# Kernel tuning notes

Measured on AMD Instinct MI355X. Metric: run time of the kernel, lower is better.

Reference implementation:

```python
import jax, jax.numpy as jnp
import numpy as np

D_MODEL = 1024
EXPAND = 2
D_INNER = D_MODEL * EXPAND  # 2048
D_STATE = 16
D_CONV = 4
B, T = 4, 2048


def setup_inputs() -> dict:
    key = jax.random.key(0)
    ks = jax.random.split(key, 8)
    s = 0.02  # small init std for numeric stability
    return {
        "x": jax.random.normal(ks[0], (B, T, D_MODEL), jnp.float32),
        "in_proj_w": jax.random.normal(ks[1], (2 * D_INNER, D_MODEL), jnp.float32) * s,
        "conv_w": jax.random.normal(ks[2], (D_INNER, 1, D_CONV), jnp.float32) * s,
        "conv_b": jnp.zeros((D_INNER,), jnp.float32),
        "x_proj_w": jax.random.normal(ks[3], (2 * D_STATE, D_INNER), jnp.float32) * s,
        "dt_proj_w": jax.random.normal(ks[4], (D_INNER, D_STATE), jnp.float32) * s,
        "dt_proj_b": jnp.zeros((D_INNER,), jnp.float32),
        "D_param": jnp.ones((D_INNER,), jnp.float32),
        "out_proj_w": jax.random.normal(ks[5], (D_MODEL, D_INNER), jnp.float32) * s,
    }


def reference(x, in_proj_w, conv_w, conv_b, x_proj_w, dt_proj_w, dt_proj_b, D_param, out_proj_w):
    Bsz, Tlen, _ = x.shape
    # in_proj (no bias), torch Linear: x @ W.T
    xz = jnp.einsum('btd,ed->bte', x, in_proj_w)            # [B,T,2*D_INNER]
    x_inner, z = jnp.split(xz, 2, axis=-1)                   # each [B,T,D_INNER]
    # depthwise causal conv1d: left-pad d_conv-1, take first T outputs
    xc = jnp.transpose(x_inner, (0, 2, 1))                   # [B,D_INNER,T]
    xc = jax.lax.conv_general_dilated(
        xc, conv_w, window_strides=(1,), padding=[(D_CONV - 1, 0)],
        feature_group_count=D_INNER)
    xc = xc + conv_b[None, :, None]
    x_conv = jax.nn.silu(jnp.transpose(xc, (0, 2, 1)))       # [B,T,D_INNER]
    # x_proj -> (B_ssm, C_ssm); C_ssm is unused by the simplified scan (faithful)
    x_ssm = jnp.einsum('btd,ed->bte', x_conv, x_proj_w)      # [B,T,2*D_STATE]
    B_ssm, C_ssm = jnp.split(x_ssm, 2, axis=-1)
    dt = jax.nn.softplus(jnp.einsum('btn,dn->btd', B_ssm, dt_proj_w) + dt_proj_b)  # [B,T,D_INNER]
    # simplified selective scan: EMA with scalar-per-timestep gate
    alpha = jax.nn.sigmoid(jnp.mean(dt, axis=-1, keepdims=True))  # [B,T,1]

    def step(h, inp):
        a, xt = inp
        h = a * h + (1.0 - a) * xt
        return h, h

    aT = jnp.transpose(alpha, (1, 0, 2))   # [T,B,1]
    xT = jnp.transpose(x_conv, (1, 0, 2))  # [T,B,D_INNER]
    h0 = jnp.zeros((Bsz, D_INNER), x.dtype)
    _, ys = jax.lax.scan(step, h0, (aT, xT))
    y = jnp.transpose(ys, (1, 0, 2))        # [B,T,D_INNER]
    y = y * D_param + x_conv                # skip with learned D
    y = y * jax.nn.silu(z)                  # gate
    out = jnp.einsum('btd,ed->bte', y, out_proj_w)  # [B,T,D_MODEL]
    return out
```

## Files before the change

### kernel.cpp

```cpp
#include <hip/hip_runtime.h>
#include <stdint.h>

#define TLEN   2048
#define DMODEL 1024
#define DINNER 2048
#define MROWS  8192
#define NCH    16
#define CHUNK  128

typedef unsigned short u16;
typedef __bf16 bf16x8 __attribute__((ext_vector_type(8)));
typedef float  f32x4  __attribute__((ext_vector_type(4)));

__device__ __forceinline__ float bf2f(u16 u) {
  union { unsigned int i; float f; } v; v.i = ((unsigned int)u) << 16; return v.f;
}
__device__ __forceinline__ u16 f2bf(float f) {
  union { float f; unsigned int u; } v; v.f = f;
  unsigned int u = v.u;
  return (u16)((u + 0x7fffu + ((u >> 16) & 1u)) >> 16);
}
__device__ __forceinline__ float silu_f(float x) { return x / (1.f + __expf(-x)); }

__device__ __forceinline__ void async16(const u16* g, u16* l) {
  __builtin_amdgcn_global_load_lds(
      (const __attribute__((address_space(1))) void*)(g),
      (__attribute__((address_space(3))) void*)(l),
      16, 0, 0);
}

#define BAR      asm volatile("s_barrier" ::: "memory")
#define WAITV(n) asm volatile("s_waitcnt vmcnt(" #n ")" ::: "memory")
#define PRIO1    __builtin_amdgcn_s_setprio(1)
#define PRIO0    __builtin_amdgcn_s_setprio(0)

__global__ __launch_bounds__(256) void k_convert(const float* __restrict__ x,
    const float* __restrict__ w1, const float* __restrict__ w3,
    const float* __restrict__ xpw,
    u16* __restrict__ xb, u16* __restrict__ w1b, u16* __restrict__ w3b,
    u16* __restrict__ xpwb) {
  int i = blockIdx.x * 256 + threadIdx.x;
  const int nx  = MROWS * DMODEL / 4;
  const int nw1 = 2 * DINNER * DMODEL / 4;
  const int nw3 = DMODEL * DINNER / 4;
  const float* src; u16* dst; int j;
  if (i < nx)                  { src = x;   dst = xb;   j = i; }
  else if (i < nx + nw1)       { src = w1;  dst = w1b;  j = i - nx; }
  else if (i < nx + nw1 + nw3) { src = w3;  dst = w3b;  j = i - nx - nw1; }
  else                         { src = xpw; dst = xpwb; j = i - nx - nw1 - nw3; }
  float4 v = ((const float4*)src)[j];
  ushort4 o;
  o.x = f2bf(v.x); o.y = f2bf(v.y); o.z = f2bf(v.z); o.w = f2bf(v.w);
  ((ushort4*)dst)[j] = o;
}

__device__ __forceinline__ u16* regp(u16* lds, int s, int mat, int h) {
  return lds + (((s * 2 + mat) * 2 + h) * 8192);
}

__device__ __forceinline__ void read_a(bf16x8 (&dst)[4][2], const u16* reg,
                                       int qa, int fr, int c0, int c1) {
  #pragma unroll
  for (int m = 0; m < 4; m++) {
    const u16* p = reg + (qa * 64 + m * 16 + fr) * 64;
    dst[m][0] = *(const bf16x8*)(p + c0);
    dst[m][1] = *(const bf16x8*)(p + c1);
  }
}
__device__ __forceinline__ void read_b(bf16x8 (&dst)[2][2], const u16* reg,
                                       int rb, int c0, int c1) {
  #pragma unroll
  for (int n = 0; n < 2; n++) {
    const u16* p = reg + (rb + n * 16) * 64;
    dst[n][0] = *(const bf16x8*)(p + c0);
    dst[n][1] = *(const bf16x8*)(p + c1);
  }
}
__device__ __forceinline__ void mfma_quad(f32x4 (&acc)[8][4],
    const bf16x8 (&af)[4][2], const bf16x8 (&bf)[2][2], int qa, int qb) {
  #pragma unroll
  for (int m = 0; m < 4; m++)
    #pragma unroll
    for (int n = 0; n < 2; n++)
      #pragma unroll
      for (int ks = 0; ks < 2; ks++)
        acc[qa * 4 + m][qb * 2 + n] = __builtin_amdgcn_mfma_f32_16x16x32_bf16(
            af[m][ks], bf[n][ks], acc[qa * 4 + m][qb * 2 + n], 0, 0, 0);
}

template<int N, int K, bool OUT_BF16>
__global__ __launch_bounds__(512) void k_gemm8p(const u16* __restrict__ A,
    const u16* __restrict__ Bm, void* __restrict__ C) {
  static_assert(K % 128 == 0, "K must be multiple of 128");
  extern __shared__ u16 lds[];
  const int tid  = threadIdx.x;
  const int lane = tid & 63;
  const int wave = tid >> 6;
  const int wm   = wave >> 2;
  const int wn   = wave & 3;
  const int fr   = lane & 15;
  const int q    = lane >> 4;

  int wg = blockIdx.x, nwg = gridDim.x, swz = wg;
  if ((nwg & 7) == 0) swz = (wg & 7) * (nwg >> 3) + (wg >> 3);
  const int NT_N = N / 256;
  const size_t blockM = (size_t)(swz / NT_N) * 256;
  const size_t blockN = (size_t)(swz % NT_N) * 256;

  const int rsub   = tid >> 3;
  const int srcCol = 8 * ((tid & 7) ^ (rsub & 7));
  const u16* gA = A  + (blockM + rsub) * (size_t)K + srcCol;
  const u16* gB = Bm + (blockN + rsub) * (size_t)K + srcCol;

#define STAGE(sl, mat, h, kt) do {                                           \
    const u16* _g = ((mat) ? gB : gA) + (size_t)(h) * (128 * (size_t)K)      \
                    + (size_t)(kt) * 64;                                     \
    u16* _l = regp(lds, (sl), (mat), (h)) + tid * 8;                         \
    async16(_g, _l);                                                         \
    async16(_g + (size_t)64 * K, _l + 4096);                                 \
  } while (0)

  const int c0 = (((q * 16)      ^ ((fr & 7) << 4)) >> 1);
  const int c1 = (((64 + q * 16) ^ ((fr & 7) << 4)) >> 1);
  const int rb = (wn & 1) * 64 + fr;

  f32x4 acc[8][4] = {};
  bf16x8 a0[4][2], a1[4][2], bl[2][2], bh[2][2];

  const int NT = K / 64;
  const int NITER = K / 128;

  STAGE(0, 0, 0, 0); STAGE(0, 0, 1, 0); STAGE(0, 1, 0, 0); STAGE(0, 1, 1, 0);
  STAGE(1, 1, 0, 1); STAGE(1, 1, 1, 1); STAGE(1, 0, 0, 1);
  WAITV(6);
  BAR;

  for (int it = 0; it < NITER; ++it) {
    const int t2 = 2 * it + 2, t3 = 2 * it + 3;
    const bool pf = (t2 < NT);
    read_a(a0, regp(lds, 0, 0, wm), 0, fr, c0, c1);
    read_b(bl, regp(lds, 0, 1, wn >> 1), rb, c0, c1);
    STAGE(1, 0, 1, 2 * it + 1);
    BAR;
    PRIO1; mfma_quad(acc, a0, bl, 0, 0); PRIO0;
    BAR;
    read_b(bh, regp(lds, 0, 1, wn >> 1), rb + 32, c0, c1);
    if (pf) STAGE(0, 1, 0, t2);
    BAR;
    PRIO1; mfma_quad(acc, a0, bh, 0, 1); PRIO0;
    BAR;
    read_a(a1, regp(lds, 0, 0, wm), 1, fr, c0, c1);
    if (pf) STAGE(0, 1, 1, t2);
    BAR;
    PRIO1; mfma_quad(acc, a1, bl, 1, 0); PRIO0;
    BAR;
    if (pf) STAGE(0, 0, 0, t2);
    BAR;
    PRIO1; mfma_quad(acc, a1, bh, 1, 1); PRIO0;
    if (pf) { WAITV(6); } else { WAITV(0); }
    BAR;
    read_a(a0, regp(lds, 1, 0, wm), 0, fr, c0, c1);
    read_b(bl, regp(lds, 1, 1, wn >> 1), rb, c0, c1);
    if (pf) STAGE(0, 0, 1, t2);
    BAR;
    PRIO1; mfma_quad(acc, a0, bl, 0, 0); PRIO0;
    BAR;
    read_b(bh, regp(lds, 1, 1, wn >> 1), rb + 32, c0, c1);
    if (pf) STAGE(1, 1, 0, t3);
    BAR;
    PRIO1; mfma_quad(acc, a0, bh, 0, 1); PRIO0;
    BAR;
    read_a(a1, regp(lds, 1, 0, wm), 1, fr, c0, c1);
    if (pf) STAGE(1, 1, 1, t3);
    BAR;
    PRIO1; mfma_quad(acc, a1, bl, 1, 0); PRIO0;
    BAR;
    if (pf) STAGE(1, 0, 0, t3);
    BAR;
    PRIO1; mfma_quad(acc, a1, bh, 1, 1); PRIO0;
    if (pf) { WAITV(6); BAR; } else { BAR; }
  }
#undef STAGE

  {
    const size_t r0  = blockM + (size_t)wm * 128;
    const size_t cc0 = blockN + (size_t)wn * 64;
    #pragma unroll
    for (int m = 0; m < 8; m++)
      #pragma unroll
      for (int n = 0; n < 4; n++)
        #pragma unroll
        for (int r = 0; r < 4; r++) {
          size_t row = r0 + m * 16 + q * 4 + r;
          size_t col = cc0 + n * 16 + fr;
          float v = acc[m][n][r];
          if (OUT_BF16) ((u16*)C)[row * N + col] = f2bf(v);
          else          ((float*)C)[row * N + col] = v;
        }
  }
}

template<int N, int K, bool OUT_BF16>
__global__ __launch_bounds__(256) void k_gemm_bt(const u16* __restrict__ A,
    const u16* __restrict__ B, void* __restrict__ C) {
  __shared__ u16 sA[2][128 * 32];
  __shared__ u16 sB[2][128 * 32];
  const int tid  = threadIdx.x;
  const int lane = tid & 63;
  const int wave = tid >> 6;
  const int wm   = (wave >> 1) * 64;
  const int wn   = (wave & 1) * 64;
  const int fr   = lane & 15;
  const int q    = lane >> 4;
  const size_t blockM = (size_t)blockIdx.y * 128;
  const size_t blockN = (size_t)blockIdx.x * 128;

  const int srow = lane >> 2;
  const int scol = (lane & 3) * 8;
  const u16* gA = A + (blockM + (size_t)wave * 32 + srow) * (size_t)K + scol;
  const u16* gB = B + (blockN + (size_t)wave * 32 + srow) * (size_t)K + scol;
  u16* lA0 = sA[0] + wave * 1024;
  u16* lA1 = sA[1] + wave * 1024;
  u16* lB0 = sB[0] + wave * 1024;
  u16* lB1 = sB[1] + wave * 1024;

  f32x4 acc[4][4] = {};

  for (int kt = 0; kt < K; kt += 64) {
    async16(gA + kt,                        lA0);
    async16(gA + 16 * (size_t)K + kt,       lA0 + 512);
    async16(gA + kt + 32,                   lA1);
    async16(gA + 16 * (size_t)K + kt + 32,  lA1 + 512);
    async16(gB + kt,                        lB0);
    async16(gB + 16 * (size_t)K + kt,       lB0 + 512);
    async16(gB + kt + 32,                   lB1);
    async16(gB + 16 * (size_t)K + kt + 32,  lB1 + 512);
    __syncthreads();

    #pragma unroll
    for (int h = 0; h < 2; h++) {
      bf16x8 af[4], bfr[4];
      #pragma unroll
      for (int tm = 0; tm < 4; tm++)
        af[tm] = *(const bf16x8*)(sA[h] + (wm + tm * 16 + fr) * 32 + q * 8);
      #pragma unroll
      for (int tn = 0; tn < 4; tn++)
        bfr[tn] = *(const bf16x8*)(sB[h] + (wn + tn * 16 + fr) * 32 + q * 8);
      #pragma unroll
      for (int tm = 0; tm < 4; tm++)
        #pragma unroll
        for (int tn = 0; tn < 4; tn++)
          acc[tm][tn] = __builtin_amdgcn_mfma_f32_16x16x32_bf16(
              af[tm], bfr[tn], acc[tm][tn], 0, 0, 0);
    }
    __syncthreads();
  }

  #pragma unroll
  for (int tm = 0; tm < 4; tm++)
    #pragma unroll
    for (int tn = 0; tn < 4; tn++)
      #pragma unroll
      for (int r = 0; r < 4; r++) {
        size_t row = blockM + wm + tm * 16 + q * 4 + r;
        size_t col = blockN + wn + tn * 16 + fr;
        float v = acc[tm][tn][r];
        if (OUT_BF16) ((u16*)C)[row * N + col] = f2bf(v);
        else          ((float*)C)[row * N + col] = v;
      }
}

__global__ __launch_bounds__(256) void k_conv(const u16* __restrict__ xz,
    const float* __restrict__ cw, const float* __restrict__ cb,
    u16* __restrict__ xc) {
  int idx = blockIdx.x * 256 + threadIdx.x;
  int d  = idx & (DINNER - 1);
  int tb = (idx >> 11) & 255;
  int b  = idx >> 19;
  float4 w = ((const float4*)cw)[d];
  float bias = cb[d];
  const u16* inp = xz + ((size_t)(b * TLEN + tb * 8)) * 4096 + d;
  float v[11];
  #pragma unroll
  for (int j = 0; j < 11; j++) {
    int t = tb * 8 - 3 + j;
    v[j] = (t >= 0) ? bf2f(inp[(ptrdiff_t)(j - 3) * 4096]) : 0.f;
  }
  u16* outp = xc + ((size_t)(b * TLEN + tb * 8)) * DINNER + d;
  #pragma unroll
  for (int i = 0; i < 8; i++) {
    float acc = bias + w.x * v[i] + w.y * v[i + 1] + w.z * v[i + 2] + w.w * v[i + 3];
    outp[(size_t)i * DINNER] = f2bf(silu_f(acc));
  }
}

__global__ __launch_bounds__(256) void k_bssm(const u16* __restrict__ xc,
    const u16* __restrict__ xpwb, float* __restrict__ bssm) {
  const int tid  = threadIdx.x;
  const int lane = tid & 63;
  const int wave = tid >> 6;
  const int fr   = lane & 15;
  const int q    = lane >> 4;
  const size_t row0 = (size_t)blockIdx.x * 32;
  const int k0 = wave * 512;

  f32x4 acc[2] = {};
  #pragma unroll
  for (int kk = 0; kk < 512; kk += 32) {
    const int kb = k0 + kk + q * 8;
    bf16x8 bfrag = *(const bf16x8*)(xpwb + (size_t)fr * DINNER + kb);
    #pragma unroll
    for (int tm = 0; tm < 2; tm++) {
      bf16x8 afrag = *(const bf16x8*)(xc + (row0 + tm * 16 + fr) * (size_t)DINNER + kb);
      acc[tm] = __builtin_amdgcn_mfma_f32_16x16x32_bf16(afrag, bfrag, acc[tm], 0, 0, 0);
    }
  }

  __shared__ float red[4][32][16];
  #pragma unroll
  for (int tm = 0; tm < 2; tm++)
    #pragma unroll
    for (int r = 0; r < 4; r++)
      red[wave][tm * 16 + q * 4 + r][fr] = acc[tm][r];
  __syncthreads();
  #pragma unroll
  for (int i = tid; i < 512; i += 256) {
    int r = i >> 4, n = i & 15;
    bssm[(row0 + r) * 16 + n] =
        red[0][r][n] + red[1][r][n] + red[2][r][n] + red[3][r][n];
  }
}

__global__ __launch_bounds__(256) void k_alpha(const float* __restrict__ bssm,
    const float* __restrict__ dtw, const float* __restrict__ dtb,
    float* __restrict__ alpha) {
  const int tid = threadIdx.x;
  const size_t row0 = (size_t)blockIdx.x * 16;
  __shared__ float4 sB[16][4];
  { int r = tid >> 4, n = tid & 15;
    ((float*)&sB[r][0])[n] = bssm[(row0 + r) * 16 + n]; }
  __syncthreads();

  float rowsum[16];
  #pragma unroll
  for (int r = 0; r < 16; r++) rowsum[r] = 0.f;

  #pragma unroll 1
  for (int m = 0; m < 4; m++) {
    const int d0 = m * 512 + tid * 2;
    float4 w[2][4]; float bias[2];
    #pragma unroll
    for (int j = 0; j < 2; j++) {
      const float4* wp = (const float4*)(dtw + (size_t)(d0 + j) * 16);
      w[j][0] = wp[0]; w[j][1] = wp[1]; w[j][2] = wp[2]; w[j][3] = wp[3];
      bias[j] = dtb[d0 + j];
    }
    #pragma unroll
    for (int r = 0; r < 16; r++) {
      float4 b0 = sB[r][0], b1 = sB[r][1], b2 = sB[r][2], b3 = sB[r][3];
      float s = 0.f;
      #pragma unroll
      for (int j = 0; j < 2; j++) {
        float dot = bias[j]
          + b0.x * w[j][0].x + b0.y * w[j][0].y + b0.z * w[j][0].z + b0.w * w[j][0].w
          + b1.x * w[j][1].x + b1.y * w[j][1].y + b1.z * w[j][1].z + b1.w * w[j][1].w
          + b2.x * w[j][2].x + b2.y * w[j][2].y + b2.z * w[j][2].z + b2.w * w[j][2].w
          + b3.x * w[j][3].x + b3.y * w[j][3].y + b3.z * w[j][3].z + b3.w * w[j][3].w;
        s += (dot > 15.f) ? dot : __logf(1.f + __expf(dot));
      }
      rowsum[r] += s;
    }
  }
  #pragma unroll
  for (int r = 0; r < 16; r++)
    #pragma unroll
    for (int off = 32; off > 0; off >>= 1) rowsum[r] += __shfl_xor(rowsum[r], off);
  __shared__ float red[4][16];
  if ((tid & 63) == 0) {
    #pragma unroll
    for (int r = 0; r < 16; r++) red[tid >> 6][r] = rowsum[r];
  }
  __syncthreads();
  if (tid < 16) {
    float mean = (red[0][tid] + red[1][tid] + red[2][tid] + red[3][tid]) * (1.f / DINNER);
    alpha[row0 + tid] = 1.f / (1.f + __expf(-mean));
  }
}

__global__ __launch_bounds__(256) void k_scan1(const u16* __restrict__ xc,
    const float* __restrict__ alpha, float* __restrict__ carry) {
  const int blk = blockIdx.x;
  const int g = blk & 7;
  const int c = (blk >> 3) & 15;
  const int b = blk >> 7;
  const int d = g * 256 + threadIdx.x;
  __shared__ float sa[CHUNK];
  if (threadIdx.x < CHUNK) sa[threadIdx.x] = alpha[b * TLEN + c * CHUNK + threadIdx.x];
  __syncthreads();
  const u16* xp = xc + ((size_t)(b * TLEN + c * CHUNK)) * DINNER + d;
  float h = 0.f;
  #pragma unroll 8
  for (int i = 0; i < CHUNK; i++) {
    float a = sa[i];
    float xv = bf2f(xp[(size_t)i * DINNER]);
    h = a * h + (1.f - a) * xv;
  }
  carry[((size_t)(b * NCH + c)) * DINNER + d] = h;
}

__global__ __launch_bounds__(256) void k_scan2(float* __restrict__ carry,
    const float* __restrict__ alpha) {
  int i = blockIdx.x * 256 + threadIdx.x;
  int b = i >> 11;
  int d = i & (DINNER - 1);
  __shared__ float sP[NCH];
  if (threadIdx.x < NCH) {
    const float* ap = alpha + b * TLEN + threadIdx.x * CHUNK;
    float p = 1.f;
    for (int j = 0; j < CHUNK; j++) p *= ap[j];
    sP[threadIdx.x] = p;
  }
  __syncthreads();
  float h = 0.f;
  #pragma unroll
  for (int c = 0; c < NCH; c++) {
    size_t idx = ((size_t)(b * NCH + c)) * DINNER + d;
    float cv = carry[idx];
    carry[idx] = h;
    h = sP[c] * h + cv;
  }
}

__global__ __launch_bounds__(256) void k_scan3(const u16* __restrict__ xc,
    const u16* __restrict__ xz, const float* __restrict__ alpha,
    const float* __restrict__ Hs, const float* __restrict__ Dp,
    u16* __restrict__ yg) {
  const int blk = blockIdx.x;
  const int g = blk & 7;
  const int c = (blk >> 3) & 15;
  const int b = blk >> 7;
  const int d = g * 256 + threadIdx.x;
  __shared__ float sa[CHUNK];
  if (threadIdx.x < CHUNK) sa[threadIdx.x] = alpha[b * TLEN + c * CHUNK + threadIdx.x];
  __syncthreads();
  float h = Hs[((size_t)(b * NCH + c)) * DINNER + d];
  const float Dv = Dp[d];
  const size_t row0 = (size_t)(b * TLEN + c * CHUNK);
  #pragma unroll 4
  for (int i = 0; i < CHUNK; i++) {
    size_t row = row0 + i;
    float a = sa[i];
    float xv = bf2f(xc[row * DINNER + d]);
    h = a * h + (1.f - a) * xv;
    float zv = bf2f(xz[row * 4096 + DINNER + d]);
    float y = h * Dv + xv;
    yg[row * DINNER + d] = f2bf(y * silu_f(zv));
  }
}

extern "C" void kernel_launch(void* const* d_in, const int* in_sizes, int n_in,
                              void* d_out, int out_size, void* d_ws, size_t ws_size,
                              hipStream_t stream) {
  const float* x   = (const float*)d_in[0];
  const float* w1  = (const float*)d_in[1];
  const float* cw  = (const float*)d_in[2];
  const float* cb  = (const float*)d_in[3];
  const float* xpw = (const float*)d_in[4];
  const float* dtw = (const float*)d_in[5];
  const float* dtb = (const float*)d_in[6];
  const float* Dp  = (const float*)d_in[7];
  const float* w3  = (const float*)d_in[8];
  float* out = (float*)d_out;
  char* ws = (char*)d_ws;

  u16*   xb    = (u16*)(ws + 0);
  u16*   w1b   = (u16*)(ws + 16777216);
  u16*   w3b   = (u16*)(ws + 25165824);
  u16*   xz    = (u16*)(ws + 29360128);
  u16*   xc    = (u16*)(ws + 96468992);
  u16*   yg    = (u16*)(ws + 130023424);
  float* bssm  = (float*)(ws + 163577856);
  float* alpha = (float*)(ws + 164102144);
  float* carry = (float*)(ws + 164135168);
  u16*   xpwb  = (u16*)(ws + 164659456);

  k_convert<<<14368, 256, 0, stream>>>(x, w1, w3, xpw, xb, w1b, w3b, xpwb);
  k_gemm8p<4096, 1024, true><<<512, 512, 131072, stream>>>(xb, w1b, xz);
  k_conv   <<<8192, 256, 0, stream>>>(xz, cw, cb, xc);
  k_bssm   <<<256, 256, 0, stream>>>(xc, xpwb, bssm);
  k_alpha  <<<512, 256, 0, stream>>>(bssm, dtw, dtb, alpha);
  k_scan1  <<<512, 256, 0, stream>>>(xc, alpha, carry);
  k_scan2  <<<32, 256, 0, stream>>>(carry, alpha);
  k_scan3  <<<512, 256, 0, stream>>>(xc, xz, alpha, carry, Dp, yg);
  k_gemm_bt<1024, 2048, false><<<dim3(8, 64), 256, 0, stream>>>(yg, w3b, out);
}
```

Before: 329.8 us.

## Vectorize conv and scan kernels, shorten scan chunks, split-K output GEMM

Conv, scan1 and scan3 now process 8 consecutive channels per thread with 16-byte bf16 loads and stores instead of scalar 2-byte accesses. Scan chunk length shrinks from 128 to 32, giving more chunks and shorter serial chains. The output projection GEMM uses 512 threads with two K halves reduced through shared memory to raise occupancy and latency hiding. The carry buffer is moved to reuse the dead input-conversion region; fewer threads in scans may reduce parallelism.

```diff
diff --git a/kernel.cpp b/kernel.cpp
--- a/kernel.cpp
+++ b/kernel.cpp
@@ -5,8 +5,8 @@
 #define DMODEL 1024
 #define DINNER 2048
 #define MROWS  8192
-#define NCH    16
-#define CHUNK  128
+#define NCH    64
+#define CHUNK  32
 
 typedef unsigned short u16;
 typedef __bf16 bf16x8 __attribute__((ext_vector_type(8)));
@@ -201,32 +201,34 @@
 }
 
 template<int N, int K, bool OUT_BF16>
-__global__ __launch_bounds__(256) void k_gemm_bt(const u16* __restrict__ A,
+__global__ __launch_bounds__(512) void k_gemm_sk(const u16* __restrict__ A,
     const u16* __restrict__ B, void* __restrict__ C) {
-  __shared__ u16 sA[2][128 * 32];
-  __shared__ u16 sB[2][128 * 32];
-  const int tid  = threadIdx.x;
-  const int lane = tid & 63;
-  const int wave = tid >> 6;
-  const int wm   = (wave >> 1) * 64;
-  const int wn   = (wave & 1) * 64;
-  const int fr   = lane & 15;
-  const int q    = lane >> 4;
+  __shared__ u16 smem[2][2][2][4096];
+  const int tid   = threadIdx.x;
+  const int lane  = tid & 63;
+  const int wave8 = tid >> 6;
+  const int kw    = wave8 >> 2;
+  const int wave  = wave8 & 3;
+  const int wm    = (wave >> 1) * 64;
+  const int wn    = (wave & 1) * 64;
+  const int fr    = lane & 15;
+  const int q     = lane >> 4;
   const size_t blockM = (size_t)blockIdx.y * 128;
   const size_t blockN = (size_t)blockIdx.x * 128;
 
   const int srow = lane >> 2;
   const int scol = (lane & 3) * 8;
-  const u16* gA = A + (blockM + (size_t)wave * 32 + srow) * (size_t)K + scol;
-  const u16* gB = B + (blockN + (size_t)wave * 32 + srow) * (size_t)K + scol;
-  u16* lA0 = sA[0] + wave * 1024;
-  u16* lA1 = sA[1] + wave * 1024;
-  u16* lB0 = sB[0] + wave * 1024;
-  u16* lB1 = sB[1] + wave * 1024;
+  const size_t kbase = (size_t)kw * (K / 2);
+  const u16* gA = A + (blockM + (size_t)wave * 32 + srow) * (size_t)K + kbase + scol;
+  const u16* gB = B + (blockN + (size_t)wave * 32 + srow) * (size_t)K + kbase + scol;
+  u16* lA0 = smem[kw][0][0] + wave * 1024;
+  u16* lA1 = smem[kw][0][1] + wave * 1024;
+  u16* lB0 = smem[kw][1][0] + wave * 1024;
+  u16* lB1 = smem[kw][1][1] + wave * 1024;
 
   f32x4 acc[4][4] = {};
 
-  for (int kt = 0; kt < K; kt += 64) {
+  for (int kt = 0; kt < K / 2; kt += 64) {
     async16(gA + kt,                        lA0);
     async16(gA + 16 * (size_t)K + kt,       lA0 + 512);
     async16(gA + kt + 32,                   lA1);
@@ -242,10 +244,10 @@
       bf16x8 af[4], bfr[4];
       #pragma unroll
       for (int tm = 0; tm < 4; tm++)
-        af[tm] = *(const bf16x8*)(sA[h] + (wm + tm * 16 + fr) * 32 + q * 8);
+        af[tm] = *(const bf16x8*)(smem[kw][0][h] + (wm + tm * 16 + fr) * 32 + q * 8);
       #pragma unroll
       for (int tn = 0; tn < 4; tn++)
-        bfr[tn] = *(const bf16x8*)(sB[h] + (wn + tn * 16 + fr) * 32 + q * 8);
+        bfr[tn] = *(const bf16x8*)(smem[kw][1][h] + (wn + tn * 16 + fr) * 32 + q * 8);
       #pragma unroll
       for (int tm = 0; tm < 4; tm++)
         #pragma unroll
@@ -256,41 +258,82 @@
     __syncthreads();
   }
 
-  #pragma unroll
-  for (int tm = 0; tm < 4; tm++)
-    #pragma unroll
-    for (int tn = 0; tn < 4; tn++)
-      #pragma unroll
-      for (int r = 0; r < 4; r++) {
-        size_t row = blockM + wm + tm * 16 + q * 4 + r;
-        size_t col = blockN + wn + tn * 16 + fr;
-        float v = acc[tm][tn][r];
-        if (OUT_BF16) ((u16*)C)[row * N + col] = f2bf(v);
-        else          ((float*)C)[row * N + col] = v;
-      }
+  float* red = (float*)smem;
+  if (kw == 1) {
+    const int t2 = tid - 256;
+    #pragma unroll
+    for (int tm = 0; tm < 4; tm++)
+      #pragma unroll
+      for (int tn = 0; tn < 4; tn++)
+        #pragma unroll
+        for (int r = 0; r < 4; r++)
+          red[((t2 * 4 + tm) * 4 + tn) * 4 + r] = acc[tm][tn][r];
+  }
+  __syncthreads();
+  if (kw == 0) {
+    #pragma unroll
+    for (int tm = 0; tm < 4; tm++)
+      #pragma unroll
+      for (int tn = 0; tn < 4; tn++)
+        #pragma unroll
+        for (int r = 0; r < 4; r++) {
+          float v = acc[tm][tn][r] + red[((tid * 4 + tm) * 4 + tn) * 4 + r];
+          size_t row = blockM + wm + tm * 16 + q * 4 + r;
+          size_t col = blockN + wn + tn * 16 + fr;
+          if (OUT_BF16) ((u16*)C)[row * N + col] = f2bf(v);
+          else          ((float*)C)[row * N + col] = v;
+        }
+  }
 }
 
 __global__ __launch_bounds__(256) void k_conv(const u16* __restrict__ xz,
     const float* __restrict__ cw, const float* __restrict__ cb,
     u16* __restrict__ xc) {
-  int idx = blockIdx.x * 256 + threadIdx.x;
-  int d  = idx & (DINNER - 1);
-  int tb = (idx >> 11) & 255;
-  int b  = idx >> 19;
-  float4 w = ((const float4*)cw)[d];
-  float bias = cb[d];
-  const u16* inp = xz + ((size_t)(b * TLEN + tb * 8)) * 4096 + d;
-  float v[11];
-  #pragma unroll
-  for (int j = 0; j < 11; j++) {
-    int t = tb * 8 - 3 + j;
-    v[j] = (t >= 0) ? bf2f(inp[(ptrdiff_t)(j - 3) * 4096]) : 0.f;
-  }
-  u16* outp = xc + ((size_t)(b * TLEN + tb * 8)) * DINNER + d;
+  const int tb = blockIdx.x & 255;
+  const int b  = blockIdx.x >> 8;
+  const int d0 = threadIdx.x * 8;
+
+  float wgt[8][4], bias[8];
+  #pragma unroll
+  for (int j = 0; j < 8; j++) {
+    float4 wv = ((const float4*)cw)[d0 + j];
+    wgt[j][0] = wv.x; wgt[j][1] = wv.y; wgt[j][2] = wv.z; wgt[j][3] = wv.w;
+    bias[j] = cb[d0 + j];
+  }
+
+  const int t0 = tb * 8;
+  const u16* base = xz + ((size_t)(b * TLEN + t0)) * 4096 + d0;
+  float win[3][8];
+  #pragma unroll
+  for (int k = 0; k < 3; k++) {
+    const int t = t0 - 3 + k;
+    if (t >= 0) {
+      bf16x8 v = *(const bf16x8*)(base + (ptrdiff_t)(k - 3) * 4096);
+      #pragma unroll
+      for (int j = 0; j < 8; j++) win[k][j] = bf2f(((u16*)&v)[j]);
+    } else {
+      #pragma unroll
+      for (int j = 0; j < 8; j++) win[k][j] = 0.f;
+    }
+  }
+
+  u16* outp = xc + ((size_t)(b * TLEN + t0)) * DINNER + d0;
   #pragma unroll
   for (int i = 0; i < 8; i++) {
-    float acc = bias + w.x * v[i] + w.y * v[i + 1] + w.z * v[i + 2] + w.w * v[i + 3];
-    outp[(size_t)i * DINNER] = f2bf(silu_f(acc));
+    bf16x8 v = *(const bf16x8*)(base + (ptrdiff_t)i * 4096);
+    float cur[8];
+    #pragma unroll
+    for (int j = 0; j < 8; j++) cur[j] = bf2f(((u16*)&v)[j]);
+    union { u16 a[8]; int4 v4; } o;
+    #pragma unroll
+    for (int j = 0; j < 8; j++) {
+      float acc = bias[j] + wgt[j][0] * win[0][j] + wgt[j][1] * win[1][j]
+                + wgt[j][2] * win[2][j] + wgt[j][3] * cur[j];
+      o.a[j] = f2bf(silu_f(acc));
+    }
+    *(int4*)(outp + (size_t)i * DINNER) = o.v4;
+    #pragma unroll
+    for (int j = 0; j < 8; j++) { win[0][j] = win[1][j]; win[1][j] = win[2][j]; win[2][j] = cur[j]; }
   }
 }
 
@@ -389,23 +432,26 @@
 
 __global__ __launch_bounds__(256) void k_scan1(const u16* __restrict__ xc,
     const float* __restrict__ alpha, float* __restrict__ carry) {
-  const int blk = blockIdx.x;
-  const int g = blk & 7;
-  const int c = (blk >> 3) & 15;
-  const int b = blk >> 7;
-  const int d = g * 256 + threadIdx.x;
+  const int c = blockIdx.x & 63;
+  const int b = blockIdx.x >> 6;
+  const int d0 = threadIdx.x * 8;
   __shared__ float sa[CHUNK];
   if (threadIdx.x < CHUNK) sa[threadIdx.x] = alpha[b * TLEN + c * CHUNK + threadIdx.x];
   __syncthreads();
-  const u16* xp = xc + ((size_t)(b * TLEN + c * CHUNK)) * DINNER + d;
-  float h = 0.f;
-  #pragma unroll 8
+  const u16* xp = xc + ((size_t)(b * TLEN + c * CHUNK)) * DINNER + d0;
+  float h[8];
+  #pragma unroll
+  for (int j = 0; j < 8; j++) h[j] = 0.f;
+  #pragma unroll 4
   for (int i = 0; i < CHUNK; i++) {
+    bf16x8 v = *(const bf16x8*)(xp + (size_t)i * DINNER);
     float a = sa[i];
-    float xv = bf2f(xp[(size_t)i * DINNER]);
-    h = a * h + (1.f - a) * xv;
-  }
-  carry[((size_t)(b * NCH + c)) * DINNER + d] = h;
+    #pragma unroll
+    for (int j = 0; j < 8; j++) h[j] = a * h[j] + (1.f - a) * bf2f(((u16*)&v)[j]);
+  }
+  float* cp = carry + ((size_t)(b * NCH + c)) * DINNER + d0;
+  #pragma unroll
+  for (int j = 0; j < 8; j++) cp[j] = h[j];
 }
 
 __global__ __launch_bounds__(256) void k_scan2(float* __restrict__ carry,
@@ -435,26 +481,33 @@
     const u16* __restrict__ xz, const float* __restrict__ alpha,
     const float* __restrict__ Hs, const float* __restrict__ Dp,
     u16* __restrict__ yg) {
-  const int blk = blockIdx.x;
-  const int g = blk & 7;
-  const int c = (blk >> 3) & 15;
-  const int b = blk >> 7;
-  const int d = g * 256 + threadIdx.x;
+  const int c = blockIdx.x & 63;
+  const int b = blockIdx.x >> 6;
+  const int d0 = threadIdx.x * 8;
   __shared__ float sa[CHUNK];
   if (threadIdx.x < CHUNK) sa[threadIdx.x] = alpha[b * TLEN + c * CHUNK + threadIdx.x];
   __syncthreads();
-  float h = Hs[((size_t)(b * NCH + c)) * DINNER + d];
-  const float Dv = Dp[d];
+  float h[8], Dv[8];
+  { const float* hp = Hs + ((size_t)(b * NCH + c)) * DINNER + d0;
+    #pragma unroll
+    for (int j = 0; j < 8; j++) { h[j] = hp[j]; Dv[j] = Dp[d0 + j]; } }
   const size_t row0 = (size_t)(b * TLEN + c * CHUNK);
-  #pragma unroll 4
+  #pragma unroll 2
   for (int i = 0; i < CHUNK; i++) {
-    size_t row = row0 + i;
-    float a = sa[i];
-    float xv = bf2f(xc[row * DINNER + d]);
-    h = a * h + (1.f - a) * xv;
-    float zv = bf2f(xz[row * 4096 + DINNER + d]);
-    float y = h * Dv + xv;
-    yg[row * DINNER + d] = f2bf(y * silu_f(zv));
+    const size_t row = row0 + i;
+    bf16x8 xv8 = *(const bf16x8*)(xc + row * DINNER + d0);
+    bf16x8 zv8 = *(const bf16x8*)(xz + row * 4096 + DINNER + d0);
+    const float a = sa[i];
+    union { u16 o[8]; int4 v4; } out;
+    #pragma unroll
+    for (int j = 0; j < 8; j++) {
+      float xv = bf2f(((u16*)&xv8)[j]);
+      float zv = bf2f(((u16*)&zv8)[j]);
+      h[j] = a * h[j] + (1.f - a) * xv;
+      float y = h[j] * Dv[j] + xv;
+      out.o[j] = f2bf(y * silu_f(zv));
+    }
+    *(int4*)(yg + row * DINNER + d0) = out.v4;
   }
 }
 
@@ -481,16 +534,16 @@
   u16*   yg    = (u16*)(ws + 130023424);
   float* bssm  = (float*)(ws + 163577856);
   float* alpha = (float*)(ws + 164102144);
-  float* carry = (float*)(ws + 164135168);
+  float* carry = (float*)(ws + 0);
   u16*   xpwb  = (u16*)(ws + 164659456);
 
   k_convert<<<14368, 256, 0, stream>>>(x, w1, w3, xpw, xb, w1b, w3b, xpwb);
   k_gemm8p<4096, 1024, true><<<512, 512, 131072, stream>>>(xb, w1b, xz);
-  k_conv   <<<8192, 256, 0, stream>>>(xz, cw, cb, xc);
+  k_conv   <<<1024, 256, 0, stream>>>(xz, cw, cb, xc);
   k_bssm   <<<256, 256, 0, stream>>>(xc, xpwb, bssm);
   k_alpha  <<<512, 256, 0, stream>>>(bssm, dtw, dtb, alpha);
-  k_scan1  <<<512, 256, 0, stream>>>(xc, alpha, carry);
+  k_scan1  <<<256, 256, 0, stream>>>(xc, alpha, carry);
   k_scan2  <<<32, 256, 0, stream>>>(carry, alpha);
-  k_scan3  <<<512, 256, 0, stream>>>(xc, xz, alpha, carry, Dp, yg);
-  k_gemm_bt<1024, 2048, false><<<dim3(8, 64), 256, 0, stream>>>(yg, w3b, out);
-}
+  k_scan3  <<<256, 256, 0, stream>>>(xc, xz, alpha, carry, Dp, yg);
+  k_gemm_sk<1024, 2048, false><<<dim3(8, 64), 512, 0, stream>>>(yg, w3b, out);
+}
```

New measurement: 327.7 us. About the same (-0.6%).
